# Performance work log

Hardware: AMD Instinct MI355X
Metric: run time of the kernel (lower is better)

## Reference

```python
import jax, jax.numpy as jnp
import numpy as np

D_MODEL = 2048
NUM_Q_HEADS = 32
NUM_KV_HEADS = 8
HEAD_SIZE = 64
GROUP_SIZE = NUM_Q_HEADS // NUM_KV_HEADS
B, T = 2, 2048


def setup_inputs() -> dict:
    key = jax.random.key(0)
    k0, k1, k2, k3 = jax.random.split(key, 4)
    std = 1.0 / np.sqrt(D_MODEL)
    x = jax.random.normal(k0, (B, T, D_MODEL), dtype=jnp.float32)
    Wq = jax.random.normal(k1, (D_MODEL, NUM_Q_HEADS * HEAD_SIZE), dtype=jnp.float32) * std
    Wk = jax.random.normal(k2, (D_MODEL, NUM_KV_HEADS * HEAD_SIZE), dtype=jnp.float32) * std
    Wv = jax.random.normal(k3, (D_MODEL, NUM_KV_HEADS * HEAD_SIZE), dtype=jnp.float32) * std
    return {"x": x, "Wq": Wq, "Wk": Wk, "Wv": Wv}


def reference(x, Wq, Wk, Wv):
    Bs, Ts, _ = x.shape
    scale = jnp.sqrt(jnp.asarray(HEAD_SIZE, dtype=x.dtype))
    # projections -> [B, H, T, D]
    q = (x @ Wq).reshape(Bs, Ts, NUM_Q_HEADS, HEAD_SIZE).transpose(0, 2, 1, 3)
    k = (x @ Wk).reshape(Bs, Ts, NUM_KV_HEADS, HEAD_SIZE).transpose(0, 2, 1, 3)
    v = (x @ Wv).reshape(Bs, Ts, NUM_KV_HEADS, HEAD_SIZE).transpose(0, 2, 1, 3)
    # repeat kv heads to match q heads (GQA)
    k = jnp.repeat(k, GROUP_SIZE, axis=1)  # [B, Hq, T, D]
    v = jnp.repeat(v, GROUP_SIZE, axis=1)
    scores = jnp.einsum('bhqd,bhkd->bhqk', q, k) / scale  # [B, Hq, T, T]
    causal = jnp.tril(jnp.ones((Ts, Ts), dtype=bool))
    scores = jnp.where(causal, scores, -jnp.inf)
    attn = jax.nn.softmax(scores, axis=-1)
    out = jnp.einsum('bhqk,bhkd->bhqd', attn, v)  # [B, Hq, T, D]
    return out.transpose(0, 2, 1, 3).reshape(Bs, Ts, NUM_Q_HEADS * HEAD_SIZE)
```

## Files before the change

kernel.cpp:

```cpp
#include <hip/hip_runtime.h>

typedef float floatx4 __attribute__((ext_vector_type(4)));
typedef short shortx8 __attribute__((ext_vector_type(8)));

#define T_SEQ 2048
#define NQH   32
#define NKVH  8
#define HD    64
#define DM    2048
#define NTOT  3072

#if __has_builtin(__builtin_amdgcn_exp2f)
#define EXP2F(x) __builtin_amdgcn_exp2f(x)
#else
#define EXP2F(x) exp2f(x)
#endif

__device__ __forceinline__ unsigned short f2bf(float f) {
    unsigned int u = __builtin_bit_cast(unsigned int, f);
    u += 0x7FFFu + ((u >> 16) & 1u);
    return (unsigned short)(u >> 16);
}
__device__ __forceinline__ unsigned int pk2bf(float a, float b) {
    return (unsigned int)f2bf(a) | ((unsigned int)f2bf(b) << 16);
}

__device__ __forceinline__ unsigned int cvtpk_bf16(float lo, float hi) {
    unsigned int r;
    asm("v_cvt_pk_bf16_f32 %0, %1, %2" : "=v"(r) : "v"(lo), "v"(hi));
    return r;
}

__device__ __forceinline__ void dma16(const unsigned short* g, unsigned short* l) {
    __builtin_amdgcn_global_load_lds(
        (const __attribute__((address_space(1))) unsigned int*)g,
        (__attribute__((address_space(3))) unsigned int*)l,
        16, 0, 0);
}

__global__ __launch_bounds__(256) void cvt_fused(
    const float* __restrict__ x, const float* __restrict__ Wq,
    const float* __restrict__ Wk, const float* __restrict__ Wv,
    unsigned short* __restrict__ xb, unsigned short* __restrict__ wt)
{
    __shared__ __align__(16) unsigned short Ts[64 * 64];
    const int id = blockIdx.x;
    const int t = threadIdx.x;
    if (id < 4096) {
        size_t i = ((size_t)id * 256 + t) * 8;
        float4 a = *(const float4*)(x + i);
        float4 b = *(const float4*)(x + i + 4);
        uint4 o;
        o.x = pk2bf(a.x, a.y); o.y = pk2bf(a.z, a.w);
        o.z = pk2bf(b.x, b.y); o.w = pk2bf(b.z, b.w);
        *(uint4*)(xb + i) = o;
        return;
    }
    const int id2 = id - 4096;
    const int k0 = (id2 & 31) * 64, n0g = (id2 >> 5) * 64;
    const float* W; int ldW, col0;
    if (n0g < 2048)      { W = Wq; ldW = 2048; col0 = n0g; }
    else if (n0g < 2560) { W = Wk; ldW = 512;  col0 = n0g - 2048; }
    else                 { W = Wv; ldW = 512;  col0 = n0g - 2560; }
    {
        const int R = t >> 3, C = (t & 7) * 8;
        const float* src0 = W + (size_t)(k0 + 2 * R) * ldW + col0 + C;
        const float* src1 = src0 + ldW;
        float4 a0 = *(const float4*)(src0);
        float4 a1 = *(const float4*)(src0 + 4);
        float4 b0 = *(const float4*)(src1);
        float4 b1 = *(const float4*)(src1 + 4);
        float lo[8] = {a0.x, a0.y, a0.z, a0.w, a1.x, a1.y, a1.z, a1.w};
        float hi[8] = {b0.x, b0.y, b0.z, b0.w, b1.x, b1.y, b1.z, b1.w};
        const int g = R >> 2;
        const int ko = (2 * R) & 7;
        #pragma unroll
        for (int i = 0; i < 8; i++) {
            const int n = C + i;
            const int gp = g ^ ((n >> 3) & 7);
            *(unsigned int*)&Ts[n * 64 + gp * 8 + ko] = pk2bf(lo[i], hi[i]);
        }
    }
    __syncthreads();
    {
        const int n = t >> 2, kc = (t & 3) * 16;
        const int f = (n >> 3) & 7;
        const int g0 = kc >> 3;
        uint4 o0 = *(const uint4*)&Ts[n * 64 + ((g0)     ^ f) * 8];
        uint4 o1 = *(const uint4*)&Ts[n * 64 + ((g0 + 1) ^ f) * 8];
        unsigned short* d = wt + (size_t)(n0g + n) * DM + k0 + kc;
        *(uint4*)d = o0; *(uint4*)(d + 8) = o1;
    }
}

__global__ __launch_bounds__(256, 4) void qkv_gemm(
    const unsigned short* __restrict__ xb,
    const unsigned short* __restrict__ wt,
    unsigned short* __restrict__ Qws, unsigned short* __restrict__ Kws,
    unsigned short* __restrict__ Vws)
{
    __shared__ __align__(16) unsigned short At[128 * 64];
    __shared__ __align__(16) unsigned short Bt[128 * 64];

    const int tid = threadIdx.x;
    const int wave = tid >> 6, lane = tid & 63;
    const int l16 = lane & 15, qd = lane >> 4;

    const int id  = blockIdx.y * 24 + blockIdx.x;
    const int xcd = id & 7, j = id >> 3;
    const int m0 = (xcd * 4 + (j & 3)) * 128;
    const int n0 = (j >> 2) * 128;

    const int mh = (wave >> 1) * 64, nh = (wave & 1) * 64;

    const int lrow = lane >> 3;
    const int cgw  = (lane & 7) ^ lrow;
    const int cg0  = (qd ^ (l16 & 7)) * 8;
    const int cg1  = ((4 | qd) ^ (l16 & 7)) * 8;

    floatx4 acc[4][4];
    #pragma unroll
    for (int mi = 0; mi < 4; mi++)
        #pragma unroll
        for (int ni = 0; ni < 4; ni++)
            acc[mi][ni] = (floatx4){0.f, 0.f, 0.f, 0.f};

    size_t gA[4], gB[4];
    int lofs[4];
    #pragma unroll
    for (int jj = 0; jj < 4; jj++) {
        const int rb = wave * 32 + jj * 8;
        gA[jj] = (size_t)(m0 + rb + lrow) * DM + cgw * 8;
        gB[jj] = (size_t)(n0 + rb + lrow) * DM + cgw * 8;
        lofs[jj] = rb * 64;
    }

    #pragma unroll
    for (int jj = 0; jj < 4; jj++) {
        dma16(xb + gA[jj], &At[lofs[jj]]);
        dma16(wt + gB[jj], &Bt[lofs[jj]]);
    }

    for (int k0 = 0; k0 < DM; k0 += 64) {
        __syncthreads();
        #pragma unroll
        for (int ks = 0; ks < 2; ks++) {
            const int cg = ks ? cg1 : cg0;
            shortx8 af[4], bfr[4];
            #pragma unroll
            for (int i = 0; i < 4; i++) {
                af[i]  = *(const shortx8*)&At[(mh + i * 16 + l16) * 64 + cg];
                bfr[i] = *(const shortx8*)&Bt[(nh + i * 16 + l16) * 64 + cg];
            }
            #pragma unroll
            for (int mi = 0; mi < 4; mi++)
                #pragma unroll
                for (int ni = 0; ni < 4; ni++)
                    acc[mi][ni] = __builtin_amdgcn_mfma_f32_16x16x32_bf16(
                        af[mi], bfr[ni], acc[mi][ni], 0, 0, 0);
        }
        __syncthreads();
        if (k0 + 64 < DM) {
            #pragma unroll
            for (int jj = 0; jj < 4; jj++) {
                dma16(xb + gA[jj] + k0 + 64, &At[lofs[jj]]);
                dma16(wt + gB[jj] + k0 + 64, &Bt[lofs[jj]]);
            }
        }
    }

    int ncol, H; unsigned short* dst; float sc; bool vtrans;
    if (n0 < 2048)      { ncol = n0;        dst = Qws; H = NQH;  sc = 0.125f * 1.44269504f; vtrans = false; }
    else if (n0 < 2560) { ncol = n0 - 2048; dst = Kws; H = NKVH; sc = 1.0f; vtrans = false; }
    else                { ncol = n0 - 2560; dst = Vws; H = NKVH; sc = 1.0f; vtrans = true;  }

    #pragma unroll
    for (int mi = 0; mi < 4; mi++)
        #pragma unroll
        for (int ni = 0; ni < 4; ni++)
            #pragma unroll
            for (int r = 0; r < 4; r++) {
                int m  = m0 + mh + mi * 16 + qd * 4 + r;
                int nc = ncol + nh + ni * 16 + l16;
                int b  = m >> 11, t = m & (T_SEQ - 1);
                int hh = nc >> 6, d = nc & 63;
                float v = acc[mi][ni][r] * sc;
                size_t idx = vtrans
                    ? ((((size_t)b * H + hh) * HD + d) << 11) + t
                    : ((((size_t)b * H + hh) * T_SEQ + t) << 6) + d;
                dst[idx] = f2bf(v);
            }
}

__global__ __launch_bounds__(512, 4) void attn_fwd(
    const unsigned short* __restrict__ Qws,
    const unsigned short* __restrict__ Kws,
    const unsigned short* __restrict__ Vtws,
    float* __restrict__ out)
{
    __shared__ __align__(16) unsigned short Ks[2][64 * 64];
    __shared__ __align__(16) unsigned short Vt[2][64 * 64];
    __shared__ __align__(16) unsigned short Ps[8][32][40];

    const int tid = threadIdx.x;
    const int wave = tid >> 6, lane = tid & 63;
    const int whead = wave & 3, wrow = wave >> 2;
    const int l16 = lane & 15, qd = lane >> 4;
    const int b = blockIdx.z;
    const int qt = b ? blockIdx.x : (31 - blockIdx.x);
    const int kh = blockIdx.y;
    const int h = kh * 4 + whead;
    const int q0 = qt * 64;
    const int mh = wrow * 32;

    const size_t qbase  = (((size_t)b * NQH + h) * T_SEQ + q0) * HD;
    const size_t kbase  = ((size_t)b * NKVH + kh) * (size_t)T_SEQ * HD;
    const size_t vtbase = ((size_t)b * NKVH + kh) * (size_t)HD * T_SEQ;

    shortx8 qfr[2][2];
    #pragma unroll
    for (int mqt = 0; mqt < 2; mqt++)
        #pragma unroll
        for (int ks = 0; ks < 2; ks++)
            qfr[mqt][ks] = *(const shortx8*)(Qws + qbase +
                (size_t)(mh + mqt * 16 + l16) * HD + ks * 32 + qd * 8);

    const shortx8 ones = {0x3F80, 0x3F80, 0x3F80, 0x3F80,
                          0x3F80, 0x3F80, 0x3F80, 0x3F80};

    floatx4 oaccT[2][4];
    #pragma unroll
    for (int mqt = 0; mqt < 2; mqt++)
        #pragma unroll
        for (int dt = 0; dt < 4; dt++)
            oaccT[mqt][dt] = (floatx4){0.f, 0.f, 0.f, 0.f};
    floatx4 psum[2];
    psum[0] = (floatx4){0.f, 0.f, 0.f, 0.f};
    psum[1] = (floatx4){0.f, 0.f, 0.f, 0.f};

    const int lrow = lane >> 3;
    const int cgw  = (lane & 7) ^ lrow;
    const int xr   = l16 & 7;
    const int rb   = wave * 8;

    dma16(Kws  + kbase  + (size_t)(rb + lrow) * HD + cgw * 8, &Ks[0][rb * 64]);
    dma16(Vtws + vtbase + (size_t)(rb + lrow) * T_SEQ + cgw * 8, &Vt[0][rb * 64]);

    for (int c = 0; c <= qt; c++) {
        const int cur = c & 1;
        __syncthreads();
        if (c < qt) {
            const int j0n = (c + 1) * 64;
            dma16(Kws  + kbase  + (size_t)(j0n + rb + lrow) * HD + cgw * 8,
                  &Ks[cur ^ 1][rb * 64]);
            dma16(Vtws + vtbase + (size_t)(rb + lrow) * T_SEQ + j0n + cgw * 8,
                  &Vt[cur ^ 1][rb * 64]);
        }

        const bool diag = (c == qt);

        #pragma unroll
        for (int kp = 0; kp < 2; kp++) {
            if (!(diag && wrow == 0 && kp == 1)) {
                shortx8 kf[2][2];
                #pragma unroll
                for (int ktl = 0; ktl < 2; ktl++) {
                    const int krow = ((kp * 2 + ktl) * 16 + l16) * 64;
                    kf[ktl][0] = *(const shortx8*)&Ks[cur][krow + ((qd ^ xr) * 8)];
                    kf[ktl][1] = *(const shortx8*)&Ks[cur][krow + (((4 | qd) ^ xr) * 8)];
                }

                const bool msk = diag && (wrow == kp);

                #pragma unroll
                for (int ktl = 0; ktl < 2; ktl++) {
                    #pragma unroll
                    for (int mqt = 0; mqt < 2; mqt++) {
                        floatx4 s = (floatx4){0.f, 0.f, 0.f, 0.f};
                        s = __builtin_amdgcn_mfma_f32_16x16x32_bf16(kf[ktl][0], qfr[mqt][0], s, 0, 0, 0);
                        s = __builtin_amdgcn_mfma_f32_16x16x32_bf16(kf[ktl][1], qfr[mqt][1], s, 0, 0, 0);
                        float pe[4];
                        #pragma unroll
                        for (int r = 0; r < 4; r++) pe[r] = EXP2F(s[r]);
                        if (msk) {
                            const int qrel  = mh + mqt * 16 + l16;
                            const int jbase = kp * 32 + ktl * 16 + qd * 4;
                            #pragma unroll
                            for (int r = 0; r < 4; r++)
                                if (jbase + r > qrel) pe[r] = 0.f;
                        }
                        uint2 dw;
                        dw.x = cvtpk_bf16(pe[0], pe[1]);
                        dw.y = cvtpk_bf16(pe[2], pe[3]);
                        *(uint2*)&Ps[wave][mqt * 16 + l16][ktl * 16 + qd * 4] = dw;
                    }
                }

                shortx8 pfr[2];
                #pragma unroll
                for (int mqt = 0; mqt < 2; mqt++)
                    pfr[mqt] = *(const shortx8*)&Ps[wave][mqt * 16 + l16][qd * 8];

                #pragma unroll
                for (int mqt = 0; mqt < 2; mqt++)
                    psum[mqt] = __builtin_amdgcn_mfma_f32_16x16x32_bf16(
                        ones, pfr[mqt], psum[mqt], 0, 0, 0);

                __builtin_amdgcn_s_setprio(1);
                #pragma unroll
                for (int dt = 0; dt < 4; dt++) {
                    const shortx8 vf = *(const shortx8*)
                        &Vt[cur][(dt * 16 + l16) * 64 + (((kp * 4 + qd) ^ xr) * 8)];
                    #pragma unroll
                    for (int mqt = 0; mqt < 2; mqt++)
                        oaccT[mqt][dt] = __builtin_amdgcn_mfma_f32_16x16x32_bf16(
                            vf, pfr[mqt], oaccT[mqt][dt], 0, 0, 0);
                }
                __builtin_amdgcn_s_setprio(0);
            }
        }
    }

    float inv[2];
    inv[0] = 1.f / psum[0][0];
    inv[1] = 1.f / psum[1][0];

    #pragma unroll
    for (int mqt = 0; mqt < 2; mqt++) {
        const int t = q0 + mh + mqt * 16 + l16;
        float* orow = out + ((size_t)b * T_SEQ + t) * (NQH * HD) + h * HD + qd * 4;
        #pragma unroll
        for (int dt = 0; dt < 4; dt++) {
            float4 o;
            o.x = oaccT[mqt][dt][0] * inv[mqt];
            o.y = oaccT[mqt][dt][1] * inv[mqt];
            o.z = oaccT[mqt][dt][2] * inv[mqt];
            o.w = oaccT[mqt][dt][3] * inv[mqt];
            *(float4*)(orow + dt * 16) = o;
        }
    }
}

extern "C" void kernel_launch(void* const* d_in, const int* in_sizes, int n_in,
                              void* d_out, int out_size, void* d_ws, size_t ws_size,
                              hipStream_t stream) {
    const float* x  = (const float*)d_in[0];
    const float* Wq = (const float*)d_in[1];
    const float* Wk = (const float*)d_in[2];
    const float* Wv = (const float*)d_in[3];
    float* out = (float*)d_out;

    unsigned short* xb  = (unsigned short*)d_out;
    unsigned short* wt  = (unsigned short*)d_ws;
    unsigned short* Qws = wt  + (size_t)NTOT * DM;
    unsigned short* Kws = Qws + (size_t)2 * NQH * T_SEQ * HD;
    unsigned short* Vws = Kws + (size_t)2 * NKVH * T_SEQ * HD;

    cvt_fused<<<4096 + 1536, 256, 0, stream>>>(x, Wq, Wk, Wv, xb, wt);
    qkv_gemm <<<dim3(24, 32), 256, 0, stream>>>(xb, wt, Qws, Kws, Vws);
    attn_fwd <<<dim3(32, NKVH, 2), 512, 0, stream>>>(Qws, Kws, Vws, out);
}
```

Before: 207.4 us.

## Fuse x fp32-to-bf16 conversion into QKV GEMM A-tile loading

Removes the separate conversion pass of x to bf16 and has the QKV GEMM read fp32 x directly, converting to bf16 in registers and writing to LDS. It uses register prefetch of the next A tile overlapped with MFMA compute. This eliminates a full read/write pass of x (about 32MB fp32 read plus 16MB write), but each GEMM block now reads fp32 A tiles, doubling A traffic across the 24 N-tile blocks sharing rows, and it raises register pressure.

```diff
diff --git a/kernel.cpp b/kernel.cpp
--- a/kernel.cpp
+++ b/kernel.cpp
@@ -38,25 +38,13 @@
         16, 0, 0);
 }
 
-__global__ __launch_bounds__(256) void cvt_fused(
-    const float* __restrict__ x, const float* __restrict__ Wq,
-    const float* __restrict__ Wk, const float* __restrict__ Wv,
-    unsigned short* __restrict__ xb, unsigned short* __restrict__ wt)
+__global__ __launch_bounds__(256) void cvt_w(
+    const float* __restrict__ Wq, const float* __restrict__ Wk,
+    const float* __restrict__ Wv, unsigned short* __restrict__ wt)
 {
     __shared__ __align__(16) unsigned short Ts[64 * 64];
-    const int id = blockIdx.x;
+    const int id2 = blockIdx.x;
     const int t = threadIdx.x;
-    if (id < 4096) {
-        size_t i = ((size_t)id * 256 + t) * 8;
-        float4 a = *(const float4*)(x + i);
-        float4 b = *(const float4*)(x + i + 4);
-        uint4 o;
-        o.x = pk2bf(a.x, a.y); o.y = pk2bf(a.z, a.w);
-        o.z = pk2bf(b.x, b.y); o.w = pk2bf(b.z, b.w);
-        *(uint4*)(xb + i) = o;
-        return;
-    }
-    const int id2 = id - 4096;
     const int k0 = (id2 & 31) * 64, n0g = (id2 >> 5) * 64;
     const float* W; int ldW, col0;
     if (n0g < 2048)      { W = Wq; ldW = 2048; col0 = n0g; }
@@ -94,7 +82,7 @@
 }
 
 __global__ __launch_bounds__(256, 4) void qkv_gemm(
-    const unsigned short* __restrict__ xb,
+    const float* __restrict__ x,
     const unsigned short* __restrict__ wt,
     unsigned short* __restrict__ Qws, unsigned short* __restrict__ Kws,
     unsigned short* __restrict__ Vws)
@@ -135,14 +123,31 @@
         lofs[jj] = rb * 64;
     }
 
-    #pragma unroll
-    for (int jj = 0; jj < 4; jj++) {
-        dma16(xb + gA[jj], &At[lofs[jj]]);
+    float4 fa[4][2];
+
+#define LOAD_AX(k0off) { _Pragma("unroll") for (int jj = 0; jj < 4; jj++) { \
+    const float* s = x + gA[jj] + (k0off); \
+    fa[jj][0] = *(const float4*)s; \
+    fa[jj][1] = *(const float4*)(s + 4); } }
+
+#define WRITE_A() { _Pragma("unroll") for (int jj = 0; jj < 4; jj++) { \
+    uint4 o; \
+    o.x = pk2bf(fa[jj][0].x, fa[jj][0].y); \
+    o.y = pk2bf(fa[jj][0].z, fa[jj][0].w); \
+    o.z = pk2bf(fa[jj][1].x, fa[jj][1].y); \
+    o.w = pk2bf(fa[jj][1].z, fa[jj][1].w); \
+    *(uint4*)&At[lofs[jj] + lane * 8] = o; } }
+
+    LOAD_AX(0);
+    WRITE_A();
+    #pragma unroll
+    for (int jj = 0; jj < 4; jj++)
         dma16(wt + gB[jj], &Bt[lofs[jj]]);
-    }
 
     for (int k0 = 0; k0 < DM; k0 += 64) {
+        const bool pf = (k0 + 64 < DM);
         __syncthreads();
+        if (pf) LOAD_AX(k0 + 64);
         #pragma unroll
         for (int ks = 0; ks < 2; ks++) {
             const int cg = ks ? cg1 : cg0;
@@ -160,14 +165,15 @@
                         af[mi], bfr[ni], acc[mi][ni], 0, 0, 0);
         }
         __syncthreads();
-        if (k0 + 64 < DM) {
+        if (pf) {
+            WRITE_A();
             #pragma unroll
-            for (int jj = 0; jj < 4; jj++) {
-                dma16(xb + gA[jj] + k0 + 64, &At[lofs[jj]]);
+            for (int jj = 0; jj < 4; jj++)
                 dma16(wt + gB[jj] + k0 + 64, &Bt[lofs[jj]]);
-            }
-        }
-    }
+        }
+    }
+#undef LOAD_AX
+#undef WRITE_A
 
     int ncol, H; unsigned short* dst; float sc; bool vtrans;
     if (n0 < 2048)      { ncol = n0;        dst = Qws; H = NQH;  sc = 0.125f * 1.44269504f; vtrans = false; }
@@ -350,13 +356,12 @@
     const float* Wv = (const float*)d_in[3];
     float* out = (float*)d_out;
 
-    unsigned short* xb  = (unsigned short*)d_out;
     unsigned short* wt  = (unsigned short*)d_ws;
     unsigned short* Qws = wt  + (size_t)NTOT * DM;
     unsigned short* Kws = Qws + (size_t)2 * NQH * T_SEQ * HD;
     unsigned short* Vws = Kws + (size_t)2 * NKVH * T_SEQ * HD;
 
-    cvt_fused<<<4096 + 1536, 256, 0, stream>>>(x, Wq, Wk, Wv, xb, wt);
-    qkv_gemm <<<dim3(24, 32), 256, 0, stream>>>(xb, wt, Qws, Kws, Vws);
-    attn_fwd <<<dim3(32, NKVH, 2), 512, 0, stream>>>(Qws, Kws, Vws, out);
-}
+    cvt_w   <<<1536, 256, 0, stream>>>(Wq, Wk, Wv, wt);
+    qkv_gemm<<<dim3(24, 32), 256, 0, stream>>>(x, wt, Qws, Kws, Vws);
+    attn_fwd<<<dim3(32, NKVH, 2), 512, 0, stream>>>(Qws, Kws, Vws, out);
+}
```

Result: slower. 768.4 us (+270.4%).
